# Kernel optimization log

Measured on AMD Instinct MI355X. Metric: run time of the kernel, lower is better.

Reference implementation:

```python
import jax, jax.numpy as jnp
import numpy as np

GLY = 7      # rc.restype_order['G']
CA = 1       # rc.atom_order['CA']
CB = 3       # rc.atom_order['CB']
MIN_BIN, MAX_BIN, NUM_BINS = 3.25, 20.75, 15
MAX_REL_IDX = 32
MAX_REL_CHAIN = 2
LN_EPS = 1e-5


def layernorm(x, gamma, beta):
    mu = jnp.mean(x, axis=-1, keepdims=True)
    var = jnp.mean((x - mu) ** 2, axis=-1, keepdims=True)
    return (x - mu) * jax.lax.rsqrt(var + LN_EPS) * gamma + beta


def setup_inputs() -> dict:
    key = jax.random.key(0)
    ks = jax.random.split(key, 8)
    N, PAIR, MSA = 768, 128, 256
    n_chains = 4
    per = N // n_chains
    aatype = jax.random.randint(ks[0], (N,), 0, 21)
    residue_index = jnp.tile(jnp.arange(per), n_chains)
    asym_id = jnp.repeat(jnp.arange(n_chains), per)
    entity_id = jnp.repeat(jnp.array([0, 0, 1, 1]), per)
    sym_id = jnp.repeat(jnp.array([0, 1, 0, 1]), per)
    prev_pos = jax.random.normal(ks[1], (N, 37, 3), dtype=jnp.float32) * 8.0
    prev_pair = jax.random.normal(ks[2], (N, N, PAIR), dtype=jnp.float32)
    prev_msa_first_row = jax.random.normal(ks[3], (N, MSA), dtype=jnp.float32)
    w_dgram = jax.random.normal(ks[4], (NUM_BINS, PAIR), dtype=jnp.float32) * 0.05
    b_dgram = jnp.zeros((PAIR,), jnp.float32)
    g_pair = jnp.ones((PAIR,), jnp.float32)
    bt_pair = jnp.zeros((PAIR,), jnp.float32)
    g_msa = jnp.ones((MSA,), jnp.float32)
    bt_msa = jnp.zeros((MSA,), jnp.float32)
    w_rel = jax.random.normal(ks[5], (73, PAIR), dtype=jnp.float32) * 0.05
    b_rel = jnp.zeros((PAIR,), jnp.float32)
    return {
        'aatype': aatype, 'residue_index': residue_index, 'asym_id': asym_id,
        'entity_id': entity_id, 'sym_id': sym_id, 'prev_pos': prev_pos,
        'prev_pair': prev_pair, 'prev_msa_first_row': prev_msa_first_row,
        'w_dgram': w_dgram, 'b_dgram': b_dgram, 'g_pair': g_pair, 'bt_pair': bt_pair,
        'g_msa': g_msa, 'bt_msa': bt_msa, 'w_rel': w_rel, 'b_rel': b_rel,
    }


def reference(aatype, residue_index, asym_id, entity_id, sym_id,
              prev_pos, prev_pair, prev_msa_first_row,
              w_dgram, b_dgram, g_pair, bt_pair, g_msa, bt_msa, w_rel, b_rel):
    # pseudo-beta: CA for glycine, CB otherwise -> [N,3]
    is_gly = aatype == GLY
    pseudo_beta = jnp.where(is_gly[..., None], prev_pos[..., CA, :], prev_pos[..., CB, :])
    # pairwise squared distances [N,N,1] binned into a distogram [N,N,15]
    d2 = jnp.sum((pseudo_beta[:, None, :] - pseudo_beta[None, :, :]) ** 2, axis=-1, keepdims=True)
    lower = jnp.linspace(MIN_BIN, MAX_BIN, NUM_BINS) ** 2
    upper = jnp.concatenate([lower[1:], jnp.array([1e8], dtype=lower.dtype)])
    dgram = ((d2 > lower) & (d2 < upper)).astype(prev_pos.dtype)
    pair = jnp.einsum('ijb,bc->ijc', dgram, w_dgram) + b_dgram
    pair = pair + layernorm(prev_pair, g_pair, bt_pair)
    # relative position encoding (chain-relative, multimer style)
    asym_same = asym_id[:, None] == asym_id[None, :]
    offset = residue_index[:, None] - residue_index[None, :]
    clipped = jnp.clip(offset + MAX_REL_IDX, 0, 2 * MAX_REL_IDX)
    final_off = jnp.where(asym_same, clipped, 2 * MAX_REL_IDX + 1)
    rel_pos = jax.nn.one_hot(final_off, 2 * MAX_REL_IDX + 2, dtype=jnp.float32)
    entity_same = entity_id[:, None] == entity_id[None, :]
    rel_sym = sym_id[:, None] - sym_id[None, :]
    clipped_chain = jnp.clip(rel_sym + MAX_REL_CHAIN, 0, 2 * MAX_REL_CHAIN)
    final_chain = jnp.where(entity_same, clipped_chain, 2 * MAX_REL_CHAIN + 1)
    rel_chain = jax.nn.one_hot(final_chain, 2 * MAX_REL_CHAIN + 2, dtype=jnp.float32)
    rel_feat = jnp.concatenate(
        [rel_pos, entity_same.astype(jnp.float32)[..., None], rel_chain], axis=-1)  # [N,N,73]
    pair = pair + jnp.einsum('ijf,fc->ijc', rel_feat, w_rel) + b_rel
    msa = layernorm(prev_msa_first_row, g_msa, bt_msa)
    return msa, pair
```

## Files before the change

kernel.cpp:

```cpp
#include <hip/hip_runtime.h>

#define NRES 768
#define CPAIR 128
#define CMSA 256
#define TPAD 132

template <int CTRL>
__device__ __forceinline__ float dpp_rot_add(float v) {
    const int r = __builtin_amdgcn_update_dpp(
        0, __float_as_int(v), CTRL, 0xF, 0xF, true);
    return v + __int_as_float(r);
}

__global__ __launch_bounds__(256) void pair_kernel(
    const int* __restrict__ aatype,
    const int* __restrict__ residue_index,
    const int* __restrict__ asym_id,
    const int* __restrict__ entity_id,
    const int* __restrict__ sym_id,
    const float* __restrict__ prev_pos,
    const float* __restrict__ prev_pair,
    const float* __restrict__ w_dgram,
    const float* __restrict__ b_dgram,
    const float* __restrict__ g_pair,
    const float* __restrict__ bt_pair,
    const float* __restrict__ w_rel,
    const float* __restrict__ b_rel,
    float* __restrict__ out_pair)
{
    __shared__ float Dtab[16][TPAD];
    __shared__ float Etab[6][TPAD];
    __shared__ unsigned short packs[256];

    const int tid = threadIdx.x;
    const int bx  = blockIdx.x;
    const int i   = bx / 3;
    const int seg = bx - i * 3;
    const int j0  = seg * 256;

    for (int idx = tid; idx < 16 * 128; idx += 256) {
        const int r = idx >> 7, c = idx & 127;
        Dtab[r][c] = (r == 0) ? 0.0f : w_dgram[(r - 1) * 128 + c];
    }
    for (int idx = tid; idx < 6 * 128; idx += 256) {
        const int r = idx >> 7, c = idx & 127;
        const float cv = bt_pair[c] + b_dgram[c] + b_rel[c];
        const float wc = w_rel[(67 + r) * 128 + c];
        Etab[r][c] = cv + ((r < 5) ? (w_rel[66 * 128 + c] + wc) : wc);
    }

    {
        const int j  = j0 + tid;
        const int ai = (aatype[i] == 7) ? 1 : 3;
        const int aj = (aatype[j] == 7) ? 1 : 3;
        const float* pi = prev_pos + ((long)i * 37 + ai) * 3;
        const float* pj = prev_pos + ((long)j * 37 + aj) * 3;
        const float dx = pi[0] - pj[0];
        const float dy = pi[1] - pj[1];
        const float dz = pi[2] - pj[2];
        const float d2 = dx * dx + dy * dy + dz * dz;

        int bin = -1;
        #pragma unroll
        for (int b = 0; b < 15; ++b) {
            const float lo = 3.25f + 1.25f * (float)b;
            const float l2 = lo * lo;
            const float hi = lo + 1.25f;
            const float u2 = (b == 14) ? 1e8f : hi * hi;
            if (d2 > l2 && d2 < u2) bin = b;
        }

        const bool asame = asym_id[i] == asym_id[j];
        int off = residue_index[i] - residue_index[j] + 32;
        off = min(max(off, 0), 64);
        const int p = asame ? off : 65;

        const bool esame = entity_id[i] == entity_id[j];
        int ch = sym_id[i] - sym_id[j] + 2;
        ch = min(max(ch, 0), 4);
        const int eidx = esame ? ch : 5;

        packs[tid] = (unsigned short)((bin + 1) | (p << 4) | (eidx << 11));
    }

    const int lane = tid & 63;
    const int wid  = tid >> 6;
    const int g    = lane >> 4;
    const int t    = lane & 15;
    const int c0   = t * 4;
    const int c1   = c0 + 64;

    const float4 gp0 = *(const float4*)(g_pair + c0);
    const float4 gp1 = *(const float4*)(g_pair + c1);

    __syncthreads();

    const float* rowp = prev_pair + ((long)i * NRES + j0) * CPAIR;
    float*       outp = out_pair + ((long)i * NRES + j0) * CPAIR;

    #pragma unroll 2
    for (int k = 0; k < 16; ++k) {
        const int pl = (wid << 6) | (k << 2) | g;
        const unsigned int pk = packs[pl];
        const int bidx = pk & 15;
        const int p    = (pk >> 4) & 127;
        const int eidx = (pk >> 11) & 7;

        const float* xp = rowp + (long)pl * CPAIR;
        const float4 x0 = *(const float4*)(xp + c0);
        const float4 x1 = *(const float4*)(xp + c1);

        const float* wr = w_rel + p * 128;
        const float4 w0 = *(const float4*)(wr + c0);
        const float4 w1 = *(const float4*)(wr + c1);
        const float4 d0 = *(const float4*)(&Dtab[bidx][c0]);
        const float4 d1 = *(const float4*)(&Dtab[bidx][c1]);
        const float4 e0 = *(const float4*)(&Etab[eidx][c0]);
        const float4 e1 = *(const float4*)(&Etab[eidx][c1]);

        float s = ((x0.x + x0.y) + (x0.z + x0.w)) + ((x1.x + x1.y) + (x1.z + x1.w));
        float q = ((x0.x * x0.x + x0.y * x0.y) + (x0.z * x0.z + x0.w * x0.w)) +
                  ((x1.x * x1.x + x1.y * x1.y) + (x1.z * x1.z + x1.w * x1.w));
        s = dpp_rot_add<0x121>(s); q = dpp_rot_add<0x121>(q);
        s = dpp_rot_add<0x122>(s); q = dpp_rot_add<0x122>(q);
        s = dpp_rot_add<0x124>(s); q = dpp_rot_add<0x124>(q);
        s = dpp_rot_add<0x128>(s); q = dpp_rot_add<0x128>(q);

        const float mu = s * (1.0f / 128.0f);
        const float var = q * (1.0f / 128.0f) - mu * mu;
        const float rstd = rsqrtf(var + 1e-5f);

        const float v0 = x0.x - mu, v1 = x0.y - mu, v2 = x0.z - mu, v3 = x0.w - mu;
        const float v4 = x1.x - mu, v5 = x1.y - mu, v6 = x1.z - mu, v7 = x1.w - mu;

        float4 o0, o1;
        o0.x = v0 * rstd * gp0.x + (d0.x + w0.x + e0.x);
        o0.y = v1 * rstd * gp0.y + (d0.y + w0.y + e0.y);
        o0.z = v2 * rstd * gp0.z + (d0.z + w0.z + e0.z);
        o0.w = v3 * rstd * gp0.w + (d0.w + w0.w + e0.w);
        o1.x = v4 * rstd * gp1.x + (d1.x + w1.x + e1.x);
        o1.y = v5 * rstd * gp1.y + (d1.y + w1.y + e1.y);
        o1.z = v6 * rstd * gp1.z + (d1.z + w1.z + e1.z);
        o1.w = v7 * rstd * gp1.w + (d1.w + w1.w + e1.w);

        float* op = outp + (long)pl * CPAIR;
        *(float4*)(op + c0) = o0;
        *(float4*)(op + c1) = o1;
    }
}

__global__ __launch_bounds__(256) void msa_kernel(
    const float* __restrict__ prev_msa,
    const float* __restrict__ g_msa,
    const float* __restrict__ bt_msa,
    float* __restrict__ out_msa)
{
    const int lane = threadIdx.x & 63;
    const int row = (int)((blockIdx.x * blockDim.x + threadIdx.x) >> 6);
    if (row >= NRES) return;

    const int c = lane * 4;
    const long base = (long)row * CMSA + c;
    const float4 x = *(const float4*)(prev_msa + base);

    float s = (x.x + x.y) + (x.z + x.w);
    #pragma unroll
    for (int m = 32; m >= 1; m >>= 1) s += __shfl_xor(s, m);
    const float mu = s * (1.0f / 256.0f);

    const float a0 = x.x - mu, a1 = x.y - mu, a2 = x.z - mu, a3 = x.w - mu;
    float v = (a0 * a0 + a1 * a1) + (a2 * a2 + a3 * a3);
    #pragma unroll
    for (int m = 32; m >= 1; m >>= 1) v += __shfl_xor(v, m);
    const float rstd = rsqrtf(v * (1.0f / 256.0f) + 1e-5f);

    const float4 g  = *(const float4*)(g_msa  + c);
    const float4 bt = *(const float4*)(bt_msa + c);
    float4 o;
    o.x = a0 * rstd * g.x + bt.x;
    o.y = a1 * rstd * g.y + bt.y;
    o.z = a2 * rstd * g.z + bt.z;
    o.w = a3 * rstd * g.w + bt.w;
    *(float4*)(out_msa + base) = o;
}

extern "C" void kernel_launch(void* const* d_in, const int* in_sizes, int n_in,
                              void* d_out, int out_size, void* d_ws, size_t ws_size,
                              hipStream_t stream) {
    const int*   aatype        = (const int*)d_in[0];
    const int*   residue_index = (const int*)d_in[1];
    const int*   asym_id       = (const int*)d_in[2];
    const int*   entity_id     = (const int*)d_in[3];
    const int*   sym_id        = (const int*)d_in[4];
    const float* prev_pos      = (const float*)d_in[5];
    const float* prev_pair     = (const float*)d_in[6];
    const float* prev_msa      = (const float*)d_in[7];
    const float* w_dgram       = (const float*)d_in[8];
    const float* b_dgram       = (const float*)d_in[9];
    const float* g_pair        = (const float*)d_in[10];
    const float* bt_pair       = (const float*)d_in[11];
    const float* g_msa         = (const float*)d_in[12];
    const float* bt_msa        = (const float*)d_in[13];
    const float* w_rel         = (const float*)d_in[14];
    const float* b_rel         = (const float*)d_in[15];

    float* out_msa  = (float*)d_out;
    float* out_pair = out_msa + (long)NRES * CMSA;

    msa_kernel<<<(NRES * 64 + 255) / 256, 256, 0, stream>>>(
        prev_msa, g_msa, bt_msa, out_msa);

    pair_kernel<<<NRES * 3, 256, 0, stream>>>(
        aatype, residue_index, asym_id, entity_id, sym_id,
        prev_pos, prev_pair,
        w_dgram, b_dgram, g_pair, bt_pair, w_rel, b_rel,
        out_pair);
}
```

Before: 517.3 us.

## Flatten pair grid into 288-pair blocks with interleaved wave row mapping

Switches the pair kernel from one block per (row, 256-column segment) to blocks covering a flat range of 288 consecutive (i,j) pairs. The grid shrinks to N*N/288 blocks, and each wave now handles interleaved rows instead of one contiguous 64-row stripe. This spreads the shared-table setup over more work per block and may even out the block count across CUs. The cost is per-pair div/mod index computation and a second pass of the pack loop for the extra 32 entries.

```diff
diff --git a/kernel.cpp b/kernel.cpp
--- a/kernel.cpp
+++ b/kernel.cpp
@@ -4,6 +4,7 @@
 #define CPAIR 128
 #define CMSA 256
 #define TPAD 132
+#define PPB  288
 
 template <int CTRL>
 __device__ __forceinline__ float dpp_rot_add(float v) {
@@ -30,13 +31,10 @@
 {
     __shared__ float Dtab[16][TPAD];
     __shared__ float Etab[6][TPAD];
-    __shared__ unsigned short packs[256];
+    __shared__ unsigned short packs[PPB];
 
     const int tid = threadIdx.x;
-    const int bx  = blockIdx.x;
-    const int i   = bx / 3;
-    const int seg = bx - i * 3;
-    const int j0  = seg * 256;
+    const long q0 = (long)blockIdx.x * PPB;
 
     for (int idx = tid; idx < 16 * 128; idx += 256) {
         const int r = idx >> 7, c = idx & 127;
@@ -49,8 +47,11 @@
         Etab[r][c] = cv + ((r < 5) ? (w_rel[66 * 128 + c] + wc) : wc);
     }
 
-    {
-        const int j  = j0 + tid;
+    for (int u = tid; u < PPB; u += 256) {
+        const long q = q0 + u;
+        const int i = (int)(q / NRES);
+        const int j = (int)(q - (long)i * NRES);
+
         const int ai = (aatype[i] == 7) ? 1 : 3;
         const int aj = (aatype[j] == 7) ? 1 : 3;
         const float* pi = prev_pos + ((long)i * 37 + ai) * 3;
@@ -80,7 +81,7 @@
         ch = min(max(ch, 0), 4);
         const int eidx = esame ? ch : 5;
 
-        packs[tid] = (unsigned short)((bin + 1) | (p << 4) | (eidx << 11));
+        packs[u] = (unsigned short)((bin + 1) | (p << 4) | (eidx << 11));
     }
 
     const int lane = tid & 63;
@@ -95,12 +96,12 @@
 
     __syncthreads();
 
-    const float* rowp = prev_pair + ((long)i * NRES + j0) * CPAIR;
-    float*       outp = out_pair + ((long)i * NRES + j0) * CPAIR;
+    const float* rowp = prev_pair + q0 * CPAIR;
+    float*       outp = out_pair + q0 * CPAIR;
 
     #pragma unroll 2
-    for (int k = 0; k < 16; ++k) {
-        const int pl = (wid << 6) | (k << 2) | g;
+    for (int k = 0; k < 18; ++k) {
+        const int pl = (k << 4) | (wid << 2) | g;
         const unsigned int pk = packs[pl];
         const int bidx = pk & 15;
         const int p    = (pk >> 4) & 127;
@@ -119,15 +120,15 @@
         const float4 e1 = *(const float4*)(&Etab[eidx][c1]);
 
         float s = ((x0.x + x0.y) + (x0.z + x0.w)) + ((x1.x + x1.y) + (x1.z + x1.w));
-        float q = ((x0.x * x0.x + x0.y * x0.y) + (x0.z * x0.z + x0.w * x0.w)) +
-                  ((x1.x * x1.x + x1.y * x1.y) + (x1.z * x1.z + x1.w * x1.w));
-        s = dpp_rot_add<0x121>(s); q = dpp_rot_add<0x121>(q);
-        s = dpp_rot_add<0x122>(s); q = dpp_rot_add<0x122>(q);
-        s = dpp_rot_add<0x124>(s); q = dpp_rot_add<0x124>(q);
-        s = dpp_rot_add<0x128>(s); q = dpp_rot_add<0x128>(q);
+        float qq = ((x0.x * x0.x + x0.y * x0.y) + (x0.z * x0.z + x0.w * x0.w)) +
+                   ((x1.x * x1.x + x1.y * x1.y) + (x1.z * x1.z + x1.w * x1.w));
+        s = dpp_rot_add<0x121>(s); qq = dpp_rot_add<0x121>(qq);
+        s = dpp_rot_add<0x122>(s); qq = dpp_rot_add<0x122>(qq);
+        s = dpp_rot_add<0x124>(s); qq = dpp_rot_add<0x124>(qq);
+        s = dpp_rot_add<0x128>(s); qq = dpp_rot_add<0x128>(qq);
 
         const float mu = s * (1.0f / 128.0f);
-        const float var = q * (1.0f / 128.0f) - mu * mu;
+        const float var = qq * (1.0f / 128.0f) - mu * mu;
         const float rstd = rsqrtf(var + 1e-5f);
 
         const float v0 = x0.x - mu, v1 = x0.y - mu, v2 = x0.z - mu, v3 = x0.w - mu;
@@ -210,7 +211,7 @@
     msa_kernel<<<(NRES * 64 + 255) / 256, 256, 0, stream>>>(
         prev_msa, g_msa, bt_msa, out_msa);
 
-    pair_kernel<<<NRES * 3, 256, 0, stream>>>(
+    pair_kernel<<<(NRES * NRES) / PPB, 256, 0, stream>>>(
         aatype, residue_index, asym_id, entity_id, sym_id,
         prev_pos, prev_pair,
         w_dgram, b_dgram, g_pair, bt_pair, w_rel, b_rel,
```

New measurement: 537.9 us. +4.0%, slower.
